# Performance work log

Measured on AMD Instinct MI355X. Metric: run time of the kernel, lower is better.

The kernel has to match this reference:

```python
import jax, jax.numpy as jnp
import numpy as np

NG, NP = 40000, 80000
E = 150000
HID = 256; OUT = 256; H = 4; L = 2
D = HID // H  # 64
IN_G, IN_P = 128, 64
EDGE_DEFS = [(0, 1), (1, 0), (1, 1)]  # (src_type, dst_type): gene->peak, peak->gene, peak->peak
SCALE = 1.0 / float(np.sqrt(D))


def setup_inputs():
    key = jax.random.key(0)
    ks = iter(jax.random.split(key, 64))
    def nrm(shape, s=0.05):
        return jax.random.normal(next(ks), shape, dtype=jnp.float32) * s
    inp = {}
    inp['x_gene'] = jax.random.normal(next(ks), (NG, IN_G), dtype=jnp.float32)
    inp['x_peak'] = jax.random.normal(next(ks), (NP, IN_P), dtype=jnp.float32)
    def edges(ns, nd):
        return jnp.stack([jax.random.randint(next(ks), (E,), 0, ns),
                          jax.random.randint(next(ks), (E,), 0, nd)])
    inp['ei_gp'] = edges(NG, NP)
    inp['ei_pg'] = edges(NP, NG)
    inp['ei_pp'] = edges(NP, NP)
    # input projections per node type
    inp['W_in_g'] = nrm((IN_G, HID)); inp['b_in_g'] = jnp.zeros((HID,), jnp.float32)
    inp['W_in_p'] = nrm((IN_P, HID)); inp['b_in_p'] = jnp.zeros((HID,), jnp.float32)
    # HGTConv params, stacked over [layer, node_type] or [layer, edge_type]
    inp['Wk'] = nrm((L, 2, HID, HID)); inp['bk'] = jnp.zeros((L, 2, HID), jnp.float32)
    inp['Wq'] = nrm((L, 2, HID, HID)); inp['bq'] = jnp.zeros((L, 2, HID), jnp.float32)
    inp['Wv'] = nrm((L, 2, HID, HID)); inp['bv'] = jnp.zeros((L, 2, HID), jnp.float32)
    inp['a_rel'] = nrm((L, 3, H, D, D), 0.1)  # per-edge-type key transform
    inp['m_rel'] = nrm((L, 3, H, D, D), 0.1)  # per-edge-type message transform
    inp['p_rel'] = jnp.ones((L, 3, H), jnp.float32)  # relation prior
    inp['W_oc'] = nrm((L, 2, HID, HID)); inp['b_oc'] = jnp.zeros((L, 2, HID), jnp.float32)
    inp['skip'] = jnp.zeros((L, 2), jnp.float32)  # per-node-type skip logits
    # output projections per node type
    inp['W_out_g'] = nrm((HID, OUT)); inp['b_out_g'] = jnp.zeros((OUT,), jnp.float32)
    inp['W_out_p'] = nrm((HID, OUT)); inp['b_out_p'] = jnp.zeros((OUT,), jnp.float32)
    return inp


def _hgt_conv(xs, eis, Wk, bk, Wq, bq, Wv, bv, a_rel, m_rel, p_rel, W_oc, b_oc, skip):
    # xs: list of [N_t, HID] per node type; eis: list of [2, E] per edge type
    k = [(xs[t] @ Wk[t] + bk[t]).reshape(-1, H, D) for t in range(2)]
    q = [(xs[t] @ Wq[t] + bq[t]).reshape(-1, H, D) for t in range(2)]
    v = [(xs[t] @ Wv[t] + bv[t]).reshape(-1, H, D) for t in range(2)]
    logits = [[], []]; msgs = [[], []]; dsts = [[], []]
    for r, (st, dt) in enumerate(EDGE_DEFS):
        src, dst = eis[r][0], eis[r][1]
        k_t = jnp.einsum('nhd,hdf->nhf', k[st], a_rel[r])  # relation-specific keys at node level
        v_t = jnp.einsum('nhd,hdf->nhf', v[st], m_rel[r])  # relation-specific messages
        lg = jnp.einsum('ehd,ehd->eh', k_t[src], q[dt][dst]) * p_rel[r] * SCALE  # [E, H]
        logits[dt].append(lg); msgs[dt].append(v_t[src]); dsts[dt].append(dst)
    out = []
    for t in range(2):
        n = xs[t].shape[0]
        lg = jnp.concatenate(logits[t]); ms = jnp.concatenate(msgs[t]); dd = jnp.concatenate(dsts[t])
        # segment softmax over all incoming edges (across edge types) per dst node
        mx = jax.ops.segment_max(lg, dd, num_segments=n)            # [n, H]
        ex = jnp.exp(lg - mx[dd])
        den = jax.ops.segment_sum(ex, dd, num_segments=n)
        alpha = ex / den[dd]                                        # [Etot, H]
        agg = jax.ops.segment_sum(alpha[:, :, None] * ms, dd, num_segments=n).reshape(n, HID)
        o = jax.nn.gelu(agg) @ W_oc[t] + b_oc[t]
        a = jax.nn.sigmoid(skip[t])
        out.append(a * o + (1.0 - a) * xs[t])
    return out


def reference(x_gene, x_peak, ei_gp, ei_pg, ei_pp, W_in_g, b_in_g, W_in_p, b_in_p,
              Wk, bk, Wq, bq, Wv, bv, a_rel, m_rel, p_rel, W_oc, b_oc, skip,
              W_out_g, b_out_g, W_out_p, b_out_p):
    # eval mode: dropout disabled
    xs = [jax.nn.relu(x_gene @ W_in_g + b_in_g), jax.nn.relu(x_peak @ W_in_p + b_in_p)]
    eis = [ei_gp, ei_pg, ei_pp]
    for l in range(L):
        xs = _hgt_conv(xs, eis, Wk[l], bk[l], Wq[l], bq[l], Wv[l], bv[l],
                       a_rel[l], m_rel[l], p_rel[l], W_oc[l], b_oc[l], skip[l])
        xs = [jax.nn.relu(x) for x in xs]
    z_g = xs[0] @ W_out_g + b_out_g
    z_p = xs[1] @ W_out_p + b_out_p
    return z_g, z_p
```

## Files before the change

kernel.cpp:

```cpp
#include <hip/hip_runtime.h>

typedef unsigned short u16;
typedef unsigned int u32;
typedef __bf16 bf16x8 __attribute__((ext_vector_type(8)));
typedef float f32x4 __attribute__((ext_vector_type(4)));

#define AS_G __attribute__((address_space(1)))
#define AS_L __attribute__((address_space(3)))

__device__ __forceinline__ float b2f(u16 u){ union{u32 i; float f;}x; x.i=((u32)u)<<16; return x.f; }
__device__ __forceinline__ u16 f2b(float f){ union{float f; u32 i;}x; x.f=f; u32 r=(x.i+0x7FFFu+((x.i>>16)&1u))>>16; return (u16)r; }

__global__ void fill_f32(float* __restrict__ p, int n, float v){
  int i = blockIdx.x * 256 + threadIdx.x;
  if (i < n) p[i] = v;
}
__global__ void diag_f32(const int* __restrict__ flag, float* __restrict__ p, int n){
  if (flag[0] == 0) return;
  int i = blockIdx.x * 256 + threadIdx.x;
  if (i < n) p[i] = 3.0f;
}
__global__ void detect_k(const int* __restrict__ ei, int* __restrict__ mode){
  if (threadIdx.x == 0 && blockIdx.x == 0)
    mode[0] = ((ei[1] | ei[3] | ei[5] | ei[7]) == 0) ? 1 : 0;
}

__global__ void scatter_k(const int* __restrict__ ei_gp, const int* __restrict__ ei_pg,
                          const int* __restrict__ ei_pp, int E,
                          const int* __restrict__ mode,
                          int* __restrict__ cntg, int* __restrict__ cntp,
                          u32* __restrict__ slg, u32* __restrict__ slp,
                          int* __restrict__ flag)
{
  int e = blockIdx.x * 256 + threadIdx.x;
  if (e >= E) return;
  int y = blockIdx.y;
  const int* ei = (y == 0) ? ei_pg : (y == 1) ? ei_gp : ei_pp;
  u32 relbits   = (y == 0) ? (1u<<20) : (y == 1) ? 0u : (2u<<20);
  int nsrc      = (y == 1) ? 40000 : 80000;
  int ndst      = (y == 0) ? 40000 : 80000;
  int* cnt      = (y == 0) ? cntg : cntp;
  u32* slots    = (y == 0) ? slg  : slp;
  int src, dst;
  if (mode[0]){ src = ei[2*(size_t)e]; dst = ei[2*(size_t)E + 2*(size_t)e]; }
  else        { src = ei[e];           dst = ei[(size_t)E + e]; }
  if ((u32)src >= (u32)nsrc || (u32)dst >= (u32)ndst){ atomicOr(flag, 1); return; }
  int slot = atomicAdd(&cnt[dst], 1);
  if (slot < 32) slots[(size_t)dst * 32 + slot] = (u32)src | relbits;
}

template<int EPI, int F32OUT>
__global__ __launch_bounds__(512)
void gemm_bt(const u16* __restrict__ A, int lda, const u16* __restrict__ Bt,
             const float* __restrict__ bias, const u16* xres,
             const float* __restrict__ skipp, void* Cv, int ldc, int M, int K, int N)
{
  __shared__ __align__(16) u16 smem[24576];
  u16* Al = smem;
  u16* Bl = smem + 16384;
  const int tid  = threadIdx.x;
  const int lane = tid & 63;
  const int wid  = tid >> 6;
  const int wr   = wid >> 1, wc = wid & 1;
  const int row0 = blockIdx.x * 256, col0 = blockIdx.y * 128;

  f32x4 acc[4][4] = {};
  const int cr  = tid >> 3;
  const int ccs = (((tid & 7) ^ (cr & 7)) * 8);

  for (int k0 = 0; k0 < K; k0 += 64){
    #pragma unroll
    for (int i = 0; i < 4; i++){
      int grow = row0 + i*64 + cr; grow = grow < M ? grow : (M - 1);
      const u16* g = A + (size_t)grow * lda + (k0 + ccs);
      u16* l = Al + i*4096 + wid*512;
      __builtin_amdgcn_global_load_lds((const AS_G void*)g, (AS_L void*)l, 16, 0, 0);
    }
    #pragma unroll
    for (int i = 0; i < 2; i++){
      const u16* g = Bt + (size_t)(col0 + i*64 + cr) * K + (k0 + ccs);
      u16* l = Bl + i*4096 + wid*512;
      __builtin_amdgcn_global_load_lds((const AS_G void*)g, (AS_L void*)l, 16, 0, 0);
    }
    __syncthreads();
    #pragma unroll
    for (int ks = 0; ks < 2; ks++){
      bf16x8 aF[4], bF[4];
      const int ch8 = (((ks*4 + (lane >> 4)) ^ (lane & 7))) * 8;
      #pragma unroll
      for (int m = 0; m < 4; m++)
        aF[m] = *(const bf16x8*)&Al[(size_t)(wr*64 + m*16 + (lane & 15)) * 64 + ch8];
      #pragma unroll
      for (int n = 0; n < 4; n++)
        bF[n] = *(const bf16x8*)&Bl[(size_t)(wc*64 + n*16 + (lane & 15)) * 64 + ch8];
      #pragma unroll
      for (int m = 0; m < 4; m++)
        #pragma unroll
        for (int n = 0; n < 4; n++)
          acc[m][n] = __builtin_amdgcn_mfma_f32_16x16x32_bf16(aF[m], bF[n], acc[m][n], 0, 0, 0);
    }
    __syncthreads();
  }

  float ask = 0.f;
  if (EPI == 2) ask = 1.f / (1.f + __expf(-(*skipp)));

  if (F32OUT){
    #pragma unroll
    for (int n = 0; n < 4; n++){
      const int col = col0 + wc*64 + n*16 + (lane & 15);
      const float bv = bias[col];
      #pragma unroll
      for (int m = 0; m < 4; m++){
        const int rb = row0 + wr*64 + m*16 + (lane >> 4) * 4;
        #pragma unroll
        for (int j = 0; j < 4; j++){
          int row = rb + j;
          if (row < M) ((float*)Cv)[(size_t)row*ldc + col] = acc[m][n][j] + bv;
        }
      }
    }
  } else {
    #pragma unroll
    for (int chh = 0; chh < 2; chh++){
      __syncthreads();
      if (wc == chh){
        #pragma unroll
        for (int n = 0; n < 4; n++){
          const int cl = n*16 + (lane & 15);
          const int col = col0 + chh*64 + cl;
          const float bv = bias[col];
          #pragma unroll
          for (int m = 0; m < 4; m++){
            const int rlb = wr*64 + m*16 + (lane >> 4) * 4;
            #pragma unroll
            for (int j = 0; j < 4; j++){
              const int rl = rlb + j;
              float v = acc[m][n][j] + bv;
              if (EPI == 1) v = fmaxf(v, 0.f);
              if (EPI == 2){
                int row = row0 + rl;
                float xr = (row < M) ? b2f(xres[(size_t)row*256 + col]) : 0.f;
                v = ask * v + (1.f - ask) * xr;
                v = fmaxf(v, 0.f);
              }
              smem[rl*72 + cl] = f2b(v);
            }
          }
        }
      }
      __syncthreads();
      #pragma unroll
      for (int t = 0; t < 4; t++){
        int idx = t*512 + tid;
        int r = idx >> 3, cchunk = idx & 7;
        int grow = row0 + r;
        if (grow < M)
          *(bf16x8*)((u16*)Cv + (size_t)grow*ldc + col0 + chh*64 + cchunk*8) =
              *(const bf16x8*)&smem[r*72 + cchunk*8];
      }
    }
  }
}

__global__ void cvt_k(const float* __restrict__ in, u16* __restrict__ out, int n4){
  int i = blockIdx.x * 256 + threadIdx.x;
  if (i >= n4) return;
  float4 v = ((const float4*)in)[i];
  u16 o[4] = { f2b(v.x), f2b(v.y), f2b(v.z), f2b(v.w) };
  *(unsigned long long*)&out[(size_t)i*4] = *(unsigned long long*)o;
}

__global__ void transpose_k(const float* __restrict__ W, u16* __restrict__ Wt, int K, int N){
  int idx = blockIdx.x * 256 + threadIdx.x;
  if (idx >= K * N) return;
  int n = idx / K, k = idx % K;
  Wt[idx] = f2b(W[(size_t)k * N + n]);
}
__global__ void transpose10_k(const float* __restrict__ Wq, const float* __restrict__ Woc,
                              const float* __restrict__ Wog, const float* __restrict__ Wop,
                              u16* __restrict__ wqkv_g, u16* __restrict__ wqkv_p,
                              u16* __restrict__ woct, u16* __restrict__ woutt)
{
  int y = blockIdx.y;
  const float* W; u16* D;
  if (y < 4){ int l = y >> 1, t = y & 1;
              W = Wq + (size_t)y*65536;
              D = t ? (wqkv_p + (size_t)l*1280*256) : (wqkv_g + (size_t)l*768*256); }
  else if (y < 8){ W = Woc + (size_t)(y-4)*65536; D = woct + (size_t)(y-4)*65536; }
  else if (y == 8){ W = Wog; D = woutt; }
  else            { W = Wop; D = woutt + 65536; }
  int idx = blockIdx.x * 256 + threadIdx.x;
  int n = idx >> 8, k = idx & 255;
  D[(size_t)n*256 + k] = f2b(W[(size_t)k*256 + n]);
}

__global__ void fuse_rel_k(const float* __restrict__ Wk, const float* __restrict__ Wv,
                           const float* __restrict__ a_rel, const float* __restrict__ m_rel,
                           u16* __restrict__ wqkv_g, u16* __restrict__ wqkv_p)
{
  int y = blockIdx.y;
  int l = y / 6, rr = y % 6, rel = rr >> 1, kv = rr & 1;
  int st = (rel == 0) ? 0 : 1;
  const float* W    = (kv ? Wv : Wk) + (size_t)l*131072 + (size_t)st*65536;
  const float* arel = (kv ? m_rel : a_rel) + (size_t)l*49152 + (size_t)rel*16384;
  u16* base; size_t ld; int rowoff;
  if (rel == 0){ base = wqkv_g; ld = 768;  rowoff = 256 + kv*256; }
  else if (rel == 1){ base = wqkv_p; ld = 1280; rowoff = 256 + kv*256; }
  else              { base = wqkv_p; ld = 1280; rowoff = 768 + kv*256; }
  u16* dst = base + (size_t)l*ld*256 + (size_t)rowoff*256;
  int fo = threadIdx.x;
  int c  = blockIdx.x;
  int h = fo >> 6, f = fo & 63;
  const float* wrow = W + (size_t)c*256 + h*64;
  const float* arow = arel + (size_t)h*4096 + f;
  float s = 0.f;
  #pragma unroll 8
  for (int d = 0; d < 64; d++) s += wrow[d] * arow[(size_t)d*64];
  dst[(size_t)fo*256 + c] = f2b(s);
}

__global__ void fuse_bias_k(const float* __restrict__ bk, const float* __restrict__ bv,
                            const float* __restrict__ bq,
                            const float* __restrict__ a_rel, const float* __restrict__ m_rel,
                            float* __restrict__ bqkv_g, float* __restrict__ bqkv_p)
{
  int y = blockIdx.x, fo = threadIdx.x;
  if (y < 12){
    int l = y / 6, rr = y % 6, rel = rr >> 1, kv = rr & 1;
    int st = (rel == 0) ? 0 : 1;
    const float* b    = (kv ? bv : bk) + l*512 + st*256;
    const float* arel = (kv ? m_rel : a_rel) + (size_t)l*49152 + (size_t)rel*16384;
    float* base; int ld, rowoff;
    if (rel == 0){ base = bqkv_g; ld = 768;  rowoff = 256 + kv*256; }
    else if (rel == 1){ base = bqkv_p; ld = 1280; rowoff = 256 + kv*256; }
    else              { base = bqkv_p; ld = 1280; rowoff = 768 + kv*256; }
    int h = fo >> 6, f = fo & 63;
    float s = 0.f;
    for (int d = 0; d < 64; d++) s += b[h*64 + d] * arel[(size_t)h*4096 + (size_t)d*64 + f];
    base[(size_t)l*ld + rowoff + fo] = s;
  } else {
    int z = y - 12, l = z >> 1, t = z & 1;
    float* base = t ? bqkv_p : bqkv_g; int ld = t ? 1280 : 768;
    base[(size_t)l*ld + fo] = bq[(size_t)(l*2 + t)*256 + fo];
  }
}

__global__ __launch_bounds__(256)
void edge_agg_k(const int* __restrict__ cnt, const u32* __restrict__ slots,
                u16* qt, int qs,
                const u16* kb0, int st0, const u16* kb1, int st1, const u16* kb2, int st2,
                const float* __restrict__ prel, int n)
{
  int node = blockIdx.x * 4 + (threadIdx.x >> 6);
  int lane = threadIdx.x & 63;
  if (node >= n) return;
  const int h = lane >> 4;
  const int co = (h << 6) + ((lane & 15) << 2);
  const float pr0 = prel[0*4 + h] * 0.125f;
  const float pr1 = prel[1*4 + h] * 0.125f;
  const float pr2 = prel[2*4 + h] * 0.125f;

  u16* qrow = qt + (size_t)node * qs + co;
  ushort4 q4 = *(const ushort4*)qrow;
  float qv0 = b2f(q4.x), qv1 = b2f(q4.y), qv2 = b2f(q4.z), qv3 = b2f(q4.w);

  float den = 0.f, ac0 = 0.f, ac1 = 0.f, ac2 = 0.f, ac3 = 0.f;

  int deg = cnt[node]; if (deg > 32) deg = 32;
  for (int i0 = 0; i0 < deg; i0 += 4){
    int c = deg - i0; c = c < 4 ? c : 4;
    ushort4 k4[4], v4[4]; float prc[4];
    #pragma unroll
    for (int j = 0; j < 4; j++){
      if (j < c){
        u32 ent = slots[(size_t)node*32 + i0 + j];
        int rel = (int)(ent >> 20);
        int src = (int)(ent & 0xFFFFFu);
        const u16* base = (rel == 0 ? kb0 + (size_t)src*st0
                         : rel == 1 ? kb1 + (size_t)src*st1
                                    : kb2 + (size_t)src*st2) + co;
        k4[j] = *(const ushort4*)base;
        v4[j] = *(const ushort4*)(base + 256);
        prc[j] = (rel == 0 ? pr0 : (rel == 1 ? pr1 : pr2));
      }
    }
    #pragma unroll
    for (int j = 0; j < 4; j++){
      if (j < c){
        float p = b2f(k4[j].x)*qv0 + b2f(k4[j].y)*qv1 + b2f(k4[j].z)*qv2 + b2f(k4[j].w)*qv3;
        p += __shfl_xor(p, 1); p += __shfl_xor(p, 2); p += __shfl_xor(p, 4); p += __shfl_xor(p, 8);
        float e = __expf(fminf(p * prc[j], 80.f));
        den += e;
        ac0 += e*b2f(v4[j].x);
        ac1 += e*b2f(v4[j].y);
        ac2 += e*b2f(v4[j].z);
        ac3 += e*b2f(v4[j].w);
      }
    }
  }
  float inv = den > 0.f ? 1.f / den : 0.f;
  float xs[4] = { ac0*inv, ac1*inv, ac2*inv, ac3*inv };
  u16 o[4];
  #pragma unroll
  for (int j = 0; j < 4; j++){
    float x = xs[j];
    float t = tanhf(0.7978845608028654f * (x + 0.044715f * x * x * x));
    o[j] = f2b(0.5f * x * (1.f + t));
  }
  *(ushort4*)qrow = *(ushort4*)o;
}

extern "C" void kernel_launch(void* const* d_in, const int* in_sizes, int n_in,
                              void* d_out, int out_size, void* d_ws, size_t ws_size,
                              hipStream_t stream)
{
  const int NG = 40000, NP = 80000, E = 150000;
  float* outF = (float*)d_out;
  u16* out2 = (u16*)d_out;
  const int fb = (out_size + 255) / 256;

  if (n_in != 25){ fill_f32<<<fb, 256, 0, stream>>>(outF, out_size, 2.0f); return; }
  static const int EXP[25] = {5120000,5120000,300000,300000,300000,32768,256,16384,256,
                              262144,1024,262144,1024,262144,1024,98304,98304,24,
                              262144,1024,4,65536,256,65536,256};
  bool ok = true;
  for (int i = 0; i < 25; i++){
    if (i >= 2 && i <= 4) ok = ok && (in_sizes[i] == 300000 || in_sizes[i] == 600000);
    else                  ok = ok && (in_sizes[i] == EXP[i]);
  }
  if (!ok){ fill_f32<<<fb, 256, 0, stream>>>(outF, out_size, 0.0f); return; }

  const float* x_gene = (const float*)d_in[0];
  const float* x_peak = (const float*)d_in[1];
  const int* ei_gp  = (const int*)d_in[2];
  const int* ei_pg  = (const int*)d_in[3];
  const int* ei_pp  = (const int*)d_in[4];
  const float* W_in_g = (const float*)d_in[5];  const float* b_in_g = (const float*)d_in[6];
  const float* W_in_p = (const float*)d_in[7];  const float* b_in_p = (const float*)d_in[8];
  const float* Wk     = (const float*)d_in[9];  const float* bk     = (const float*)d_in[10];
  const float* Wq     = (const float*)d_in[11]; const float* bq     = (const float*)d_in[12];
  const float* Wv     = (const float*)d_in[13]; const float* bv     = (const float*)d_in[14];
  const float* a_rel  = (const float*)d_in[15]; const float* m_rel  = (const float*)d_in[16];
  const float* p_rel  = (const float*)d_in[17];
  const float* W_oc   = (const float*)d_in[18]; const float* b_oc   = (const float*)d_in[19];
  const float* skip   = (const float*)d_in[20];
  const float* W_out_g= (const float*)d_in[21]; const float* b_out_g= (const float*)d_in[22];
  const float* W_out_p= (const float*)d_in[23]; const float* b_out_p= (const float*)d_in[24];

  char* ws = (char*)d_ws; size_t off = 0;
  auto alloc = [&](size_t nbytes) -> void* {
    void* p = ws + off; off = (off + nbytes + 255) & ~(size_t)255; return p;
  };

  u16* xg    = (u16*)alloc((size_t)NG*256*2);
  u16* xp    = (u16*)alloc((size_t)NP*256*2);
  u16* qkvp  = (u16*)alloc((size_t)NP*1280*2);
  u16* wtin_g = (u16*)alloc(256*128*2);
  u16* wtin_p = (u16*)alloc(256*64*2);
  u16* wqkv_g = (u16*)alloc((size_t)2*768*256*2);
  u16* wqkv_p = (u16*)alloc((size_t)2*1280*256*2);
  u16* woct  = (u16*)alloc((size_t)4*65536*2);
  u16* woutt = (u16*)alloc((size_t)2*65536*2);
  float* bqkv_g = (float*)alloc((size_t)2*768*4);
  float* bqkv_p = (float*)alloc((size_t)2*1280*4);
  int* cntg  = (int*)alloc((size_t)NG*4);
  int* cntp  = (int*)alloc((size_t)NP*4);
  u32* slg   = (u32*)alloc((size_t)NG*32*4);
  u32* slp   = (u32*)alloc((size_t)NP*32*4);
  int* mode  = (int*)alloc(256);
  int* flag  = (int*)alloc(256);

  if (off > ws_size){ fill_f32<<<fb, 256, 0, stream>>>(outF, out_size, 1.0f); return; }

  u16* qkvg = out2;
  u16* xgb  = qkvp;
  u16* xpb  = qkvp + (size_t)NG*128;

  hipMemsetAsync(cntg, 0, (size_t)NG*4, stream);
  hipMemsetAsync(cntp, 0, (size_t)NP*4, stream);
  hipMemsetAsync(flag, 0, 4, stream);
  detect_k<<<1, 64, 0, stream>>>(ei_gp, mode);
  scatter_k<<<dim3((E + 255)/256, 3), 256, 0, stream>>>(ei_gp, ei_pg, ei_pp, E, mode,
                                                        cntg, cntp, slg, slp, flag);
  cvt_k<<<(NG*128/4 + 255)/256, 256, 0, stream>>>(x_gene, xgb, NG*128/4);
  cvt_k<<<(NP*64/4 + 255)/256, 256, 0, stream>>>(x_peak, xpb, NP*64/4);
  transpose_k<<<128, 256, 0, stream>>>(W_in_g, wtin_g, 128, 256);
  transpose_k<<<64,  256, 0, stream>>>(W_in_p, wtin_p, 64, 256);
  transpose10_k<<<dim3(256, 10), 256, 0, stream>>>(Wq, W_oc, W_out_g, W_out_p,
                                                   wqkv_g, wqkv_p, woct, woutt);
  fuse_rel_k<<<dim3(256, 12), 256, 0, stream>>>(Wk, Wv, a_rel, m_rel, wqkv_g, wqkv_p);
  fuse_bias_k<<<16, 256, 0, stream>>>(bk, bv, bq, a_rel, m_rel, bqkv_g, bqkv_p);

  dim3 gg(157, 2), gp(313, 2);
  dim3 gg7(157, 6), gp10(313, 10);

  gemm_bt<1,0><<<gg, 512, 0, stream>>>(xgb, 128, wtin_g, b_in_g, nullptr, nullptr, xg, 256, NG, 128, 256);
  gemm_bt<1,0><<<gp, 512, 0, stream>>>(xpb,  64, wtin_p, b_in_p, nullptr, nullptr, xp, 256, NP,  64, 256);

  for (int l = 0; l < 2; l++){
    const float* pr = p_rel + l*12;
    gemm_bt<0,0><<<gg7, 512, 0, stream>>>(xg, 256, wqkv_g + (size_t)l*768*256,
                                          bqkv_g + (size_t)l*768, nullptr, nullptr, qkvg, 768, NG, 256, 768);
    gemm_bt<0,0><<<gp10, 512, 0, stream>>>(xp, 256, wqkv_p + (size_t)l*1280*256,
                                          bqkv_p + (size_t)l*1280, nullptr, nullptr, qkvp, 1280, NP, 256, 1280);

    edge_agg_k<<<NG/4, 256, 0, stream>>>(cntg, slg, qkvg, 768,
                                         qkvp + 256, 1280, qkvp + 256, 1280, qkvp + 256, 1280, pr, NG);
    edge_agg_k<<<NP/4, 256, 0, stream>>>(cntp, slp, qkvp, 1280,
                                         qkvg + 256, 768, qkvg + 256, 768, qkvp + 768, 1280, pr, NP);

    gemm_bt<2,0><<<gg, 512, 0, stream>>>(qkvg, 768,  woct + (size_t)(l*2+0)*65536, b_oc + (l*2+0)*256,
                                         xg, skip + (l*2+0), xg, 256, NG, 256, 256);
    gemm_bt<2,0><<<gp, 512, 0, stream>>>(qkvp, 1280, woct + (size_t)(l*2+1)*65536, b_oc + (l*2+1)*256,
                                         xp, skip + (l*2+1), xp, 256, NP, 256, 256);
  }

  gemm_bt<0,1><<<gg, 512, 0, stream>>>(xg, 256, woutt,         b_out_g, nullptr, nullptr, outF,                  256, NG, 256, 256);
  gemm_bt<0,1><<<gp, 512, 0, stream>>>(xp, 256, woutt + 65536, b_out_p, nullptr, nullptr, outF + (size_t)NG*256, 256, NP, 256, 256);

  diag_f32<<<fb, 256, 0, stream>>>(flag, outF, out_size);
}
```

Before: 1.005 ms.

## Remap GEMM blocks per XCD for L2 reuse and merge edge aggregation launches

```diff
diff --git a/kernel.cpp b/kernel.cpp
--- a/kernel.cpp
+++ b/kernel.cpp
@@ -62,7 +62,23 @@
   const int lane = tid & 63;
   const int wid  = tid >> 6;
   const int wr   = wid >> 1, wc = wid & 1;
-  const int row0 = blockIdx.x * 256, col0 = blockIdx.y * 128;
+
+  const int NC = gridDim.x, NR = gridDim.y;
+  const int f  = blockIdx.y * NC + blockIdx.x;
+  const int NR8 = NR & ~7;
+  int c, r;
+  const int bulk = NC * NR8;
+  if (f < bulk){
+    int xcd = f & 7;
+    int j = f >> 3;
+    c = j % NC;
+    r = (j / NC) * 8 + xcd;
+  } else {
+    int f2 = f - bulk;
+    c = f2 % NC;
+    r = NR8 + f2 / NC;
+  }
+  const int row0 = r * 256, col0 = c * 128;
 
   f32x4 acc[4][4] = {};
   const int cr  = tid >> 3;
@@ -153,11 +169,11 @@
       #pragma unroll
       for (int t = 0; t < 4; t++){
         int idx = t*512 + tid;
-        int r = idx >> 3, cchunk = idx & 7;
-        int grow = row0 + r;
+        int rr2 = idx >> 3, cchunk = idx & 7;
+        int grow = row0 + rr2;
         if (grow < M)
           *(bf16x8*)((u16*)Cv + (size_t)grow*ldc + col0 + chh*64 + cchunk*8) =
-              *(const bf16x8*)&smem[r*72 + cchunk*8];
+              *(const bf16x8*)&smem[rr2*72 + cchunk*8];
       }
     }
   }
@@ -247,14 +263,24 @@
 }
 
 __global__ __launch_bounds__(256)
-void edge_agg_k(const int* __restrict__ cnt, const u32* __restrict__ slots,
-                u16* qt, int qs,
-                const u16* kb0, int st0, const u16* kb1, int st1, const u16* kb2, int st2,
-                const float* __restrict__ prel, int n)
-{
-  int node = blockIdx.x * 4 + (threadIdx.x >> 6);
+void edge_agg_k(const int* __restrict__ cntg, const u32* __restrict__ slg,
+                const int* __restrict__ cntp, const u32* __restrict__ slp,
+                u16* qkvg, u16* qkvp, const float* __restrict__ prel)
+{
+  const int NG = 40000;
+  int w = blockIdx.x * 4 + (threadIdx.x >> 6);
   int lane = threadIdx.x & 63;
-  if (node >= n) return;
+  const bool gene = w < NG;
+  const int node = gene ? w : w - NG;
+  const int* cnt = gene ? cntg : cntp;
+  const u32* slots = gene ? slg : slp;
+  u16* qt = gene ? qkvg : qkvp;
+  const int qs = gene ? 768 : 1280;
+  const u16 *kb0, *kb1, *kb2; int st0, st1, st2;
+  if (gene){ kb0 = kb1 = kb2 = qkvp + 256; st0 = st1 = st2 = 1280; }
+  else     { kb0 = qkvg + 256; st0 = 768; kb1 = qkvg + 256; st1 = 768;
+             kb2 = qkvp + 768; st2 = 1280; }
+
   const int h = lane >> 4;
   const int co = (h << 6) + ((lane & 15) << 2);
   const float pr0 = prel[0*4 + h] * 0.125f;
@@ -392,8 +418,8 @@
   fuse_rel_k<<<dim3(256, 12), 256, 0, stream>>>(Wk, Wv, a_rel, m_rel, wqkv_g, wqkv_p);
   fuse_bias_k<<<16, 256, 0, stream>>>(bk, bv, bq, a_rel, m_rel, bqkv_g, bqkv_p);
 
-  dim3 gg(157, 2), gp(313, 2);
-  dim3 gg7(157, 6), gp10(313, 10);
+  dim3 gg(2, 157), gp(2, 313);
+  dim3 gg7(6, 157), gp10(10, 313);
 
   gemm_bt<1,0><<<gg, 512, 0, stream>>>(xgb, 128, wtin_g, b_in_g, nullptr, nullptr, xg, 256, NG, 128, 256);
   gemm_bt<1,0><<<gp, 512, 0, stream>>>(xpb,  64, wtin_p, b_in_p, nullptr, nullptr, xp, 256, NP,  64, 256);
@@ -405,10 +431,7 @@
     gemm_bt<0,0><<<gp10, 512, 0, stream>>>(xp, 256, wqkv_p + (size_t)l*1280*256,
                                           bqkv_p + (size_t)l*1280, nullptr, nullptr, qkvp, 1280, NP, 256, 1280);
 
-    edge_agg_k<<<NG/4, 256, 0, stream>>>(cntg, slg, qkvg, 768,
-                                         qkvp + 256, 1280, qkvp + 256, 1280, qkvp + 256, 1280, pr, NG);
-    edge_agg_k<<<NP/4, 256, 0, stream>>>(cntp, slp, qkvp, 1280,
-                                         qkvg + 256, 768, qkvg + 256, 768, qkvp + 768, 1280, pr, NP);
+    edge_agg_k<<<(NG + NP)/4, 256, 0, stream>>>(cntg, slg, cntp, slp, qkvg, qkvp, pr);
 
     gemm_bt<2,0><<<gg, 512, 0, stream>>>(qkvg, 768,  woct + (size_t)(l*2+0)*65536, b_oc + (l*2+0)*256,
                                          xg, skip + (l*2+0), xg, 256, NG, 256, 256);
```

Measured after the change: 951.1 us. 1.06x faster.
